# Performance work log

Measured on AMD Instinct MI355X. Metric: run time of the kernel, lower is better.

## Reference

```python
import jax, jax.numpy as jnp
import numpy as np

B_SZ, SEQ = 16, 2048
VOCAB, EMBED = 50257, 128
DSTATE, HID, NCLS = 16, 256, 10
NEDGE = 8192  # edges per graph (avg degree 4)
LN_EPS = 1e-5


def setup_inputs() -> dict:
    key = jax.random.key(0)
    ks = jax.random.split(key, 12)
    tokens = jax.random.randint(ks[0], (B_SZ, SEQ), 0, VOCAB, dtype=jnp.int32)
    lengths = jnp.full((B_SZ,), SEQ, dtype=jnp.int32)  # full-length graphs
    edge_indices = jax.random.randint(ks[1], (B_SZ, 2, NEDGE), 0, SEQ, dtype=jnp.int32)
    emb = (jax.random.normal(ks[2], (VOCAB, EMBED)) * 0.02).at[0].set(0.0)  # padding_idx=0
    A_log = jax.random.normal(ks[3], (EMBED, DSTATE)) * 0.1
    B_w = jax.random.normal(ks[4], (DSTATE, EMBED)) * (1.0 / np.sqrt(EMBED))
    C_w = jax.random.normal(ks[5], (EMBED, DSTATE)) * (1.0 / np.sqrt(DSTATE))
    D_skip = jnp.ones((EMBED,))
    ln_g = jnp.ones((EMBED,))
    ln_b = jnp.zeros((EMBED,))
    Wmsg_w = jax.random.normal(ks[6], (HID, EMBED)) * (1.0 / np.sqrt(EMBED))
    Wupd_w = jax.random.normal(ks[7], (HID, EMBED + HID)) * (1.0 / np.sqrt(EMBED + HID))
    Wupd_b = jax.random.normal(ks[8], (HID,)) * 0.01
    cls_w = jax.random.normal(ks[9], (NCLS, HID)) * (1.0 / np.sqrt(HID))
    cls_b = jnp.zeros((NCLS,))
    return {"tokens": tokens, "lengths": lengths, "edge_indices": edge_indices,
            "emb": emb, "A_log": A_log, "B_w": B_w, "C_w": C_w, "D_skip": D_skip,
            "ln_g": ln_g, "ln_b": ln_b, "Wmsg_w": Wmsg_w, "Wupd_w": Wupd_w,
            "Wupd_b": Wupd_b, "cls_w": cls_w, "cls_b": cls_b}


def _ssm(x, A_log, B_w, C_w, D_skip, ln_g, ln_b):
    # x: (B, S, d_model). Diagonal SSM: h_t = h_{t-1}*exp(A) + B x_t (broadcast over d_model)
    Aexp = jnp.exp(-jnp.exp(A_log))  # (d_model, d_state)
    h0 = jnp.zeros((x.shape[0], EMBED, DSTATE), dtype=x.dtype)

    def step(h, x_t):  # x_t: (B, d_model)
        b_t = x_t @ B_w.T                            # (B, d_state)
        h = h * Aexp[None] + b_t[:, None, :]          # (B, d_model, d_state)
        y = h.mean(axis=1) @ C_w.T + D_skip * x_t     # (B, d_model)
        return h, y

    _, ys = jax.lax.scan(step, h0, jnp.swapaxes(x, 0, 1))
    out = jnp.swapaxes(ys, 0, 1)                      # (B, S, d_model)
    mu = out.mean(-1, keepdims=True)
    var = jnp.mean((out - mu) ** 2, axis=-1, keepdims=True)
    return ln_g * (out - mu) * jax.lax.rsqrt(var + LN_EPS) + ln_b


def reference(tokens, lengths, edge_indices, emb, A_log, B_w, C_w, D_skip,
              ln_g, ln_b, Wmsg_w, Wupd_w, Wupd_b, cls_w, cls_b):
    x = emb[tokens]                                   # (B, S, E)
    h = _ssm(x, A_log, B_w, C_w, D_skip, ln_g, ln_b)  # (B, S, E)
    src, dst = edge_indices[:, 0, :], edge_indices[:, 1, :]   # (B, Ne)
    h_src = jnp.take_along_axis(h, src[:, :, None], axis=1)   # (B, Ne, E)
    msgs = jnp.einsum('bed,hd->beh', h_src, Wmsg_w)            # (B, Ne, H)
    flat_dst = (jnp.arange(B_SZ, dtype=dst.dtype)[:, None] * SEQ + dst).reshape(-1)
    agg = jax.ops.segment_sum(msgs.reshape(-1, HID), flat_dst,
                              num_segments=B_SZ * SEQ).reshape(B_SZ, SEQ, HID)
    upd = jax.nn.relu(jnp.concatenate([h, agg], axis=-1) @ Wupd_w.T + Wupd_b)  # (B, S, H)
    pooled = upd.mean(axis=1)                          # (B, H)  (all lengths == SEQ)
    return pooled @ cls_w.T + cls_b                    # (B, NCLS)
```

## Files before the change

kernel.cpp:

```cpp
#include <hip/hip_runtime.h>

#define B_SZ   16
#define SEQ    2048
#define VOCAB  50257
#define EMBED  128
#define DSTATE 16
#define HID    256
#define NCLS   10
#define NEDGE  8192
#define KTR    64
#define LN_EPS 1e-5f
#define NROW   (B_SZ*SEQ)
#define BCAP   32
#define OVCAP  1024

#define PB_CAST   4096
#define PB_BUCKET (PB_CAST + 512)
#define PB_PRECM  (PB_BUCKET + 128)
#define PB_CTAB   (PB_PRECM + 16)
#define PB_TOTAL  (PB_CTAB + 1)

typedef float  f32x4 __attribute__((ext_vector_type(4)));
typedef short  s16x8 __attribute__((ext_vector_type(8)));

__device__ __forceinline__ float scrub(float x){
  return (x == x && fabsf(x) < 1e30f) ? x : 0.f;
}
__device__ __forceinline__ short f2b(float f){
  unsigned int u = __float_as_uint(f);
  unsigned int r = (u + 0x7fffu + ((u >> 16) & 1u)) >> 16;
  return (short)r;
}
__device__ __forceinline__ unsigned int pack2(float a, float b){
  return (unsigned int)(unsigned short)f2b(a)
       | ((unsigned int)(unsigned short)f2b(b) << 16);
}
__device__ __forceinline__ float lo2f(unsigned int v){ return __uint_as_float(v << 16); }
__device__ __forceinline__ float hi2f(unsigned int v){ return __uint_as_float(v & 0xffff0000u); }

__global__ __launch_bounds__(256) void k_prep(
    const int* __restrict__ tokens, const float* __restrict__ emb,
    const float* __restrict__ A_log, const float* __restrict__ B_w,
    const float* __restrict__ Wmsg, const float* __restrict__ Wupd,
    const int* __restrict__ edges,
    float* __restrict__ c_tab, short* __restrict__ Bf, float* __restrict__ MT,
    unsigned int* __restrict__ x_bf, int* __restrict__ cnt,
    unsigned short* __restrict__ bucket, int* __restrict__ ovf_cnt,
    int* __restrict__ ovf){
  int bid = blockIdx.x, tid = threadIdx.x;
  if (bid < PB_CAST){
    int gid = bid*256 + tid;
    int row = gid >> 5, ch = gid & 31;
    int tok = tokens[row];
    tok = tok < 0 ? 0 : (tok >= VOCAB ? VOCAB-1 : tok);
    float4 v = *(const float4*)(emb + (size_t)tok*EMBED + ch*4);
    uint2 o; o.x = pack2(v.x, v.y); o.y = pack2(v.z, v.w);
    *(uint2*)(x_bf + (size_t)row*(EMBED/2) + ch*2) = o;
  } else if (bid < PB_BUCKET){
    int eid = (bid-PB_CAST)*256 + tid;
    int b = eid >> 13, i = eid & (NEDGE-1);
    const int* ei = edges + (size_t)b*2*NEDGE;
    int s = ei[i]         & (SEQ-1);
    int d = ei[NEDGE + i] & (SEQ-1);
    int gdst = (b << 11) | d;
    int slot = atomicAdd(&cnt[gdst], 1);
    if (slot < BCAP) bucket[(size_t)gdst*BCAP + slot] = (unsigned short)s;
    else {
      int o = atomicAdd(ovf_cnt, 1);
      if (o < OVCAP) ovf[o] = ((b << 11) | s) | (gdst << 16);
    }
  } else if (bid < PB_PRECM){
    int hp = (bid-PB_BUCKET)*2 + (tid >> 7);
    int e  = tid & 127;
    const float* w2 = Wupd + (size_t)hp*384 + 128;
    float acc = 0.f;
    for (int h1 = 0; h1 < HID; ++h1)
      acc += Wmsg[h1*EMBED + e] * w2[h1];
    MT[(size_t)hp*EMBED + e] = scrub(acc);
  } else if (bid < PB_CTAB){
    if (tid < 64){
      int d = bid - PB_PRECM, lane = tid;
      float a0 = scrub(expf(-expf(A_log[(2*lane+0)*DSTATE + d])));
      float a1 = scrub(expf(-expf(A_log[(2*lane+1)*DSTATE + d])));
      float p0 = 1.f, p1 = 1.f;
      for (int k = 0; k < KTR; ++k){
        float s = p0 + p1;
        for (int off = 32; off; off >>= 1) s += __shfl_down(s, off);
        if (lane == 0) c_tab[k*DSTATE + d] = scrub(s * (1.0f/128.0f));
        p0 *= a0; p1 *= a1;
      }
    }
  } else {
    int idx = tid;
    int c = idx >> 6, lane = idx & 63;
    int n = lane & 15;
    int kb = c*32 + (lane >> 4)*8;
    short v[8];
    #pragma unroll
    for (int jj = 0; jj < 8; ++jj) v[jj] = f2b(B_w[(size_t)n*EMBED + kb + jj]);
    *(s16x8*)(Bf + (size_t)idx*8) = *(s16x8*)v;
  }
}

__global__ __launch_bounds__(256) void k_ssm_fused(
    const short* __restrict__ x_bf, const float* __restrict__ c_tab,
    const float* __restrict__ C_w, const float* __restrict__ D_skip,
    const float* __restrict__ ln_g, const float* __restrict__ ln_b,
    const short* __restrict__ Bf, const float* __restrict__ Wupd,
    const float* __restrict__ MT, unsigned int* __restrict__ h_out,
    short* __restrict__ Wcs){
  __shared__ float bsh[128][18];
  __shared__ float msh[64][18];
  __shared__ float Ct[DSTATE][EMBED+2];
  __shared__ float csh[KTR][DSTATE];
  int bid = blockIdx.x, tid = threadIdx.x;

  if (bid >= 512){
    int idx = (bid-512)*256 + tid;
    int c    = idx >> 10;
    int rem  = idx & 1023;
    int j    = rem >> 6;
    int lane = rem & 63;
    int n  = j*16 + (lane & 15);
    int kb = c*32 + (lane >> 4)*8;
    short v[8];
    #pragma unroll
    for (int jj = 0; jj < 8; ++jj){
      int k = kb + jj;
      float val = (k < 128) ? Wupd[(size_t)n*384 + k] : MT[(size_t)n*EMBED + (k-128)];
      v[jj] = f2b(val);
    }
    *(s16x8*)(Wcs + (size_t)idx*8) = *(s16x8*)v;
    return;
  }

  int b  = bid >> 5;
  int t0 = (bid & 31) * 64;
  for (int i = tid; i < DSTATE*EMBED; i += 256){
    int e = i >> 4, d = i & 15;
    Ct[d][e] = C_w[i];
  }
  for (int i = tid; i < KTR*DSTATE; i += 256)
    csh[i >> 4][i & 15] = c_tab[i];

  int wv = tid >> 6, lane = tid & 63;
  int m = lane & 15, lg = lane >> 4;

  const s16x8* Bp = (const s16x8*)Bf;
  #pragma unroll
  for (int tt = 0; tt < 2; ++tt){
    int tile = wv*2 + tt;
    int trow = t0 - 64 + tile*16;
    f32x4 acc = (f32x4){0.f,0.f,0.f,0.f};
    if (trow >= 0){
      const short* xrow = x_bf + ((size_t)(b*SEQ + trow + m))*EMBED + lg*8;
      #pragma unroll
      for (int c = 0; c < 4; ++c){
        s16x8 a = *(const s16x8*)(xrow + c*32);
        acc = __builtin_amdgcn_mfma_f32_16x16x32_bf16(a, Bp[c*64 + lane], acc, 0, 0, 0);
      }
    }
    #pragma unroll
    for (int r = 0; r < 4; ++r)
      bsh[tile*16 + lg*4 + r][m] = scrub(acc[r]);
  }
  __syncthreads();

  {
    int d = tid & 15;
    #pragma unroll
    for (int it = 0; it < 4; ++it){
      int q = (tid + it*256) >> 4;
      int t = t0 + q;
      int base = 64 + q;
      int kmax = (t+1 < KTR) ? t+1 : KTR;
      float acc = 0.f;
      for (int k = 0; k < kmax; ++k) acc += csh[k][d] * bsh[base-k][d];
      msh[q][d] = scrub(acc);
    }
  }
  __syncthreads();

  int e0 = lane*2;
  float2 dsk = *(const float2*)&D_skip[e0];
  float2 lgv = *(const float2*)&ln_g[e0];
  float2 lbv = *(const float2*)&ln_b[e0];
  const unsigned int* xb = (const unsigned int*)x_bf;
  for (int q = wv*16; q < wv*16+16; ++q){
    int row = b*SEQ + t0 + q;
    unsigned int xp = xb[(size_t)row*(EMBED/2) + lane];
    float x0 = lo2f(xp), x1 = hi2f(xp);
    float y0 = dsk.x*x0, y1 = dsk.y*x1;
    #pragma unroll
    for (int d = 0; d < DSTATE; ++d){
      float md = msh[q][d];
      y0 += md * Ct[d][e0];
      y1 += md * Ct[d][e0+1];
    }
    y0 = scrub(y0); y1 = scrub(y1);
    float s = y0+y1, s2 = y0*y0 + y1*y1;
    for (int off = 32; off; off >>= 1){ s += __shfl_down(s,off); s2 += __shfl_down(s2,off); }
    s = __shfl(s, 0); s2 = __shfl(s2, 0);
    float mu  = s * (1.f/EMBED);
    float var = s2 * (1.f/EMBED) - mu*mu;
    float inv = rsqrtf(fmaxf(var, 0.f) + LN_EPS);
    float o0 = scrub(lgv.x*(y0-mu)*inv + lbv.x);
    float o1 = scrub(lgv.y*(y1-mu)*inv + lbv.y);
    h_out[(size_t)row*(EMBED/2) + lane] = pack2(o0, o1);
  }
}

__global__ __launch_bounds__(256) void k_gather(
    const int* __restrict__ cnt, const unsigned short* __restrict__ bucket,
    const int* __restrict__ ovf_cnt, const int* __restrict__ ovf,
    const unsigned int* __restrict__ h, unsigned int* __restrict__ g){
  int wv = threadIdx.x >> 6, lane = threadIdx.x & 63;
  int gdst = blockIdx.x*4 + wv;
  int n = cnt[gdst]; n = n > BCAP ? BCAP : n;
  int b = gdst >> 11;
  const unsigned int* hb = h + (size_t)b*SEQ*(EMBED/2);
  const unsigned short* bk = bucket + (size_t)gdst*BCAP;
  float ax = 0.f, ay = 0.f;
  for (int i = 0; i < n; ++i){
    unsigned int v = hb[(size_t)bk[i]*(EMBED/2) + lane];
    ax += lo2f(v); ay += hi2f(v);
  }
  int on = *ovf_cnt; on = on > OVCAP ? OVCAP : on;
  for (int idx = 0; idx < on; ++idx){
    int pk = ovf[idx];
    if (((pk >> 16) & 0x7fff) == gdst){
      unsigned int v = h[(size_t)(pk & 0xffff)*(EMBED/2) + lane];
      ax += lo2f(v); ay += hi2f(v);
    }
  }
  g[(size_t)gdst*(EMBED/2) + lane] = pack2(scrub(ax), scrub(ay));
}

__global__ __launch_bounds__(256) void k_upd_mfma(
    const short* __restrict__ h, const short* __restrict__ g,
    const short* __restrict__ Wcs, const float* __restrict__ Wupd_b,
    float* __restrict__ pool){
  int tid = threadIdx.x;
  int wave = blockIdx.x*4 + (tid >> 6);
  int lane = tid & 63;
  int row0 = wave * 16;
  int b = row0 >> 11;
  int m = lane & 15, lg = lane >> 4;
  const short* hrow = h + (size_t)(row0+m)*EMBED + lg*8;
  const short* grow = g + (size_t)(row0+m)*EMBED + lg*8;

  f32x4 acc[16];
  #pragma unroll
  for (int j = 0; j < 16; ++j) acc[j] = (f32x4){0.f,0.f,0.f,0.f};

  const s16x8* Bp = (const s16x8*)Wcs;
  #pragma unroll
  for (int c = 0; c < 8; ++c){
    s16x8 a = (c < 4) ? *(const s16x8*)(hrow + c*32)
                      : *(const s16x8*)(grow + (c-4)*32);
    #pragma unroll
    for (int j = 0; j < 16; ++j){
      s16x8 bfr = Bp[(c*16 + j)*64 + lane];
      acc[j] = __builtin_amdgcn_mfma_f32_16x16x32_bf16(a, bfr, acc[j], 0, 0, 0);
    }
  }

  #pragma unroll
  for (int j = 0; j < 16; ++j){
    int n = j*16 + (lane & 15);
    float bias = Wupd_b[n];
    float v = 0.f;
    #pragma unroll
    for (int r = 0; r < 4; ++r) v += fmaxf(acc[j][r] + bias, 0.f);
    v += __shfl_down(v, 32);
    v += __shfl_down(v, 16);
    if (lane < 16) atomicAdd(&pool[b*HID + n], scrub(v));
  }
}

__global__ void k_cls(const float* __restrict__ pool, const float* __restrict__ cls_w,
                      const float* __restrict__ cls_b, float* __restrict__ out){
  int tid = threadIdx.x;
  if (tid >= B_SZ*NCLS) return;
  int b = tid / NCLS, c = tid - b*NCLS;
  const float* p = pool + b*HID;
  const float* w = cls_w + c*HID;
  float s = 0.f;
  for (int h1 = 0; h1 < HID; ++h1) s += p[h1]*w[h1];
  out[tid] = scrub(s * (1.0f/SEQ) + cls_b[c]);
}

extern "C" void kernel_launch(void* const* d_in, const int* in_sizes, int n_in,
                              void* d_out, int out_size, void* d_ws, size_t ws_size,
                              hipStream_t stream) {
  const int*   tokens = (const int*)d_in[0];
  const int*   edges  = (const int*)d_in[2];
  const float* emb    = (const float*)d_in[3];
  const float* A_log  = (const float*)d_in[4];
  const float* B_w    = (const float*)d_in[5];
  const float* C_w    = (const float*)d_in[6];
  const float* D_skip = (const float*)d_in[7];
  const float* ln_g   = (const float*)d_in[8];
  const float* ln_b   = (const float*)d_in[9];
  const float* Wmsg   = (const float*)d_in[10];
  const float* Wupd   = (const float*)d_in[11];
  const float* Wupd_b = (const float*)d_in[12];
  const float* cls_w  = (const float*)d_in[13];
  const float* cls_b  = (const float*)d_in[14];
  float* out = (float*)d_out;

  char* ws = (char*)d_ws;
  float* c_tab = (float*)ws;  ws += 16*1024;
  float* MT    = (float*)ws;  ws += (size_t)HID*EMBED*4;
  short* Wcs   = (short*)ws;  ws += (size_t)HID*HID*2;
  short* Bf    = (short*)ws;  ws += 16*1024;
  char*  zbase = ws;
  float* pool  = (float*)ws;  ws += (size_t)B_SZ*HID*4;
  int*   cnt   = (int*)ws;    ws += (size_t)NROW*4;
  int*   ovf_cnt = (int*)ws;  ws += 64;
  int*   ovf   = (int*)ws;    ws += OVCAP*4;
  size_t zlen = (size_t)((char*)ws - zbase);
  unsigned short* bucket = (unsigned short*)ws; ws += (size_t)NROW*BCAP*2;
  short* x_bf  = (short*)ws;  ws += (size_t)NROW*EMBED*2;
  short* h_bf  = (short*)ws;  ws += (size_t)NROW*EMBED*2;
  short* g_bf  = (short*)ws;  ws += (size_t)NROW*EMBED*2;

  hipMemsetAsync(zbase, 0, zlen, stream);
  hipLaunchKernelGGL(k_prep, dim3(PB_TOTAL), dim3(256), 0, stream,
                     tokens, emb, A_log, B_w, Wmsg, Wupd, edges,
                     c_tab, Bf, MT, (unsigned int*)x_bf, cnt, bucket, ovf_cnt, ovf);
  hipLaunchKernelGGL(k_ssm_fused, dim3(544), dim3(256), 0, stream,
                     x_bf, c_tab, C_w, D_skip, ln_g, ln_b, Bf, Wupd, MT,
                     (unsigned int*)h_bf, Wcs);
  hipLaunchKernelGGL(k_gather, dim3(NROW/4), dim3(256), 0, stream,
                     cnt, bucket, ovf_cnt, ovf, (const unsigned int*)h_bf,
                     (unsigned int*)g_bf);
  hipLaunchKernelGGL(k_upd_mfma, dim3(NROW/64), dim3(256), 0, stream,
                     h_bf, g_bf, Wcs, Wupd_b, pool);
  hipLaunchKernelGGL(k_cls, dim3(1), dim3(256), 0, stream, pool, cls_w, cls_b, out);
}
```

Baseline: 192.0 us.

## Fuse neighbor gather, update GEMM and classifier into one kernel

Merges the gather kernel into the MFMA update kernel: each block gathers neighbor sums for its 64 rows into shared memory in the MFMA operand layout, so the g buffer no longer makes a global round trip. The classifier is folded in through a last-block-done atomic counter, which removes two launches. In exchange the gather now uses 4 threads per row with 16-wide strided loads instead of one wave per row, so memory coalescing may get worse. The overflow mask also changes from 0x7fff to 0xffff.

```diff
diff --git a/kernel.cpp b/kernel.cpp
--- a/kernel.cpp
+++ b/kernel.cpp
@@ -210,44 +210,69 @@
   }
 }
 
-__global__ __launch_bounds__(256) void k_gather(
-    const int* __restrict__ cnt, const unsigned short* __restrict__ bucket,
+__global__ __launch_bounds__(256) void k_upd_fused(
+    const short* __restrict__ h, const int* __restrict__ cnt,
+    const unsigned short* __restrict__ bucket,
     const int* __restrict__ ovf_cnt, const int* __restrict__ ovf,
-    const unsigned int* __restrict__ h, unsigned int* __restrict__ g){
-  int wv = threadIdx.x >> 6, lane = threadIdx.x & 63;
-  int gdst = blockIdx.x*4 + wv;
-  int n = cnt[gdst]; n = n > BCAP ? BCAP : n;
-  int b = gdst >> 11;
-  const unsigned int* hb = h + (size_t)b*SEQ*(EMBED/2);
-  const unsigned short* bk = bucket + (size_t)gdst*BCAP;
-  float ax = 0.f, ay = 0.f;
-  for (int i = 0; i < n; ++i){
-    unsigned int v = hb[(size_t)bk[i]*(EMBED/2) + lane];
-    ax += lo2f(v); ay += hi2f(v);
-  }
-  int on = *ovf_cnt; on = on > OVCAP ? OVCAP : on;
-  for (int idx = 0; idx < on; ++idx){
-    int pk = ovf[idx];
-    if (((pk >> 16) & 0x7fff) == gdst){
-      unsigned int v = h[(size_t)(pk & 0xffff)*(EMBED/2) + lane];
-      ax += lo2f(v); ay += hi2f(v);
-    }
-  }
-  g[(size_t)gdst*(EMBED/2) + lane] = pack2(scrub(ax), scrub(ay));
-}
-
-__global__ __launch_bounds__(256) void k_upd_mfma(
-    const short* __restrict__ h, const short* __restrict__ g,
     const short* __restrict__ Wcs, const float* __restrict__ Wupd_b,
-    float* __restrict__ pool){
+    float* __restrict__ pool, const float* __restrict__ cls_w,
+    const float* __restrict__ cls_b, float* __restrict__ out,
+    int* __restrict__ done){
+  __shared__ short gsh[16*64*8];
+  __shared__ float psh[B_SZ*HID];
+  __shared__ int lastf;
   int tid = threadIdx.x;
-  int wave = blockIdx.x*4 + (tid >> 6);
-  int lane = tid & 63;
-  int row0 = wave * 16;
+  int row0 = blockIdx.x * 64;
   int b = row0 >> 11;
+
+  {
+    int r  = tid >> 2;
+    int t4 = tid & 3;
+    int gdst = row0 + r;
+    int n = cnt[gdst]; n = n > BCAP ? BCAP : n;
+    const unsigned short* bk = bucket + (size_t)gdst*BCAP;
+    const unsigned int* hb = (const unsigned int*)h + (size_t)b*SEQ*(EMBED/2);
+    float fx[16], fy[16];
+    #pragma unroll
+    for (int j = 0; j < 16; ++j){ fx[j]=0.f; fy[j]=0.f; }
+    for (int i = 0; i < n; ++i){
+      const unsigned int* src = hb + (size_t)bk[i]*(EMBED/2) + t4*16;
+      #pragma unroll
+      for (int j = 0; j < 16; ++j){
+        unsigned int v = src[j];
+        fx[j] += lo2f(v); fy[j] += hi2f(v);
+      }
+    }
+    int on = *ovf_cnt; on = on > OVCAP ? OVCAP : on;
+    for (int idx = 0; idx < on; ++idx){
+      int pk = ovf[idx];
+      if (((pk >> 16) & 0xffff) == gdst){
+        const unsigned int* src = (const unsigned int*)h
+            + (size_t)(pk & 0xffff)*(EMBED/2) + t4*16;
+        #pragma unroll
+        for (int j = 0; j < 16; ++j){
+          unsigned int v = src[j];
+          fx[j] += lo2f(v); fy[j] += hi2f(v);
+        }
+      }
+    }
+    unsigned int pk4[16];
+    #pragma unroll
+    for (int j = 0; j < 16; ++j) pk4[j] = pack2(scrub(fx[j]), scrub(fy[j]));
+    int w = r >> 4, m = r & 15;
+    unsigned int* gu = (unsigned int*)gsh;
+    #pragma unroll
+    for (int lg = 0; lg < 4; ++lg){
+      int slot = (w*4 + t4)*64 + lg*16 + m;
+      uint4 o = make_uint4(pk4[lg*4+0], pk4[lg*4+1], pk4[lg*4+2], pk4[lg*4+3]);
+      *(uint4*)&gu[slot*4] = o;
+    }
+  }
+  __syncthreads();
+
+  int wv = tid >> 6, lane = tid & 63;
   int m = lane & 15, lg = lane >> 4;
-  const short* hrow = h + (size_t)(row0+m)*EMBED + lg*8;
-  const short* grow = g + (size_t)(row0+m)*EMBED + lg*8;
+  const short* hrow = h + (size_t)(row0 + wv*16 + m)*EMBED + lg*8;
 
   f32x4 acc[16];
   #pragma unroll
@@ -257,7 +282,7 @@
   #pragma unroll
   for (int c = 0; c < 8; ++c){
     s16x8 a = (c < 4) ? *(const s16x8*)(hrow + c*32)
-                      : *(const s16x8*)(grow + (c-4)*32);
+                      : *(const s16x8*)&gsh[((wv*4 + (c-4))*64 + lane)*8];
     #pragma unroll
     for (int j = 0; j < 16; ++j){
       s16x8 bfr = Bp[(c*16 + j)*64 + lane];
@@ -276,18 +301,24 @@
     v += __shfl_down(v, 16);
     if (lane < 16) atomicAdd(&pool[b*HID + n], scrub(v));
   }
-}
-
-__global__ void k_cls(const float* __restrict__ pool, const float* __restrict__ cls_w,
-                      const float* __restrict__ cls_b, float* __restrict__ out){
-  int tid = threadIdx.x;
-  if (tid >= B_SZ*NCLS) return;
-  int b = tid / NCLS, c = tid - b*NCLS;
-  const float* p = pool + b*HID;
-  const float* w = cls_w + c*HID;
-  float s = 0.f;
-  for (int h1 = 0; h1 < HID; ++h1) s += p[h1]*w[h1];
-  out[tid] = scrub(s * (1.0f/SEQ) + cls_b[c]);
+
+  __threadfence();
+  __syncthreads();
+  if (tid == 0) lastf = (atomicAdd(done, 1) == (int)gridDim.x - 1) ? 1 : 0;
+  __syncthreads();
+  if (!lastf) return;
+  __threadfence();
+  for (int i = tid; i < B_SZ*HID; i += 256)
+    psh[i] = atomicAdd(&pool[i], 0.0f);
+  __syncthreads();
+  if (tid < B_SZ*NCLS){
+    int bb = tid / NCLS, cc = tid - bb*NCLS;
+    const float* p = psh + bb*HID;
+    const float* w = cls_w + cc*HID;
+    float s = 0.f;
+    for (int h1 = 0; h1 < HID; ++h1) s += p[h1]*w[h1];
+    out[tid] = scrub(s * (1.0f/SEQ) + cls_b[cc]);
+  }
 }
 
 extern "C" void kernel_launch(void* const* d_in, const int* in_sizes, int n_in,
@@ -319,11 +350,11 @@
   int*   cnt   = (int*)ws;    ws += (size_t)NROW*4;
   int*   ovf_cnt = (int*)ws;  ws += 64;
   int*   ovf   = (int*)ws;    ws += OVCAP*4;
+  int*   done  = (int*)ws;    ws += 64;
   size_t zlen = (size_t)((char*)ws - zbase);
   unsigned short* bucket = (unsigned short*)ws; ws += (size_t)NROW*BCAP*2;
   short* x_bf  = (short*)ws;  ws += (size_t)NROW*EMBED*2;
   short* h_bf  = (short*)ws;  ws += (size_t)NROW*EMBED*2;
-  short* g_bf  = (short*)ws;  ws += (size_t)NROW*EMBED*2;
 
   hipMemsetAsync(zbase, 0, zlen, stream);
   hipLaunchKernelGGL(k_prep, dim3(PB_TOTAL), dim3(256), 0, stream,
@@ -332,10 +363,7 @@
   hipLaunchKernelGGL(k_ssm_fused, dim3(544), dim3(256), 0, stream,
                      x_bf, c_tab, C_w, D_skip, ln_g, ln_b, Bf, Wupd, MT,
                      (unsigned int*)h_bf, Wcs);
-  hipLaunchKernelGGL(k_gather, dim3(NROW/4), dim3(256), 0, stream,
-                     cnt, bucket, ovf_cnt, ovf, (const unsigned int*)h_bf,
-                     (unsigned int*)g_bf);
-  hipLaunchKernelGGL(k_upd_mfma, dim3(NROW/64), dim3(256), 0, stream,
-                     h_bf, g_bf, Wcs, Wupd_b, pool);
-  hipLaunchKernelGGL(k_cls, dim3(1), dim3(256), 0, stream, pool, cls_w, cls_b, out);
-}
+  hipLaunchKernelGGL(k_upd_fused, dim3(NROW/64), dim3(256), 0, stream,
+                     h_bf, cnt, bucket, ovf_cnt, ovf, Wcs, Wupd_b,
+                     pool, cls_w, cls_b, out, done);
+}
```

After: 220.4 us. 1.15x slower.
